# Optimization experiments

Measured on AMD Instinct MI355X. Metric: run time of the kernel, lower is better.

The kernel has to match this reference:

```python
import jax, jax.numpy as jnp
import numpy as np

FLOW_ITERS = 8
DUAL_ITERS = 8
DUAL_STEP = 0.1
DUAL_MOM = 0.9
GRAPH_LAYERS = 2
BIG = 1e9


def _sparsemax(z, mask):
    # sparsemax along last axis; masked entries already hold -BIG, zeroed by mask after.
    V = z.shape[-1]
    zs = jnp.sort(z, axis=-1)[..., ::-1]
    cum = jnp.cumsum(zs, axis=-1)
    k = jnp.arange(1, V + 1, dtype=z.dtype)
    support = zs * k > (cum - 1.0)
    k_sel = jnp.sum(support.astype(jnp.int32), axis=-1, keepdims=True)
    tau = (jnp.take_along_axis(cum, k_sel - 1, axis=-1) - 1.0) / k_sel.astype(z.dtype)
    return jnp.maximum(z - tau, 0.0) * mask


def _min_cost_flow(props, demands):
    # iterative proportional flow routing: push relu(inflow - demand) along predicted proportions
    def body(flow, _):
        inflow = jnp.sum(flow, axis=1)[..., None]      # [B,V,1] inflow to each node
        adjusted = jax.nn.relu(inflow - demands)       # excess to re-route
        return props * adjusted, None                  # row i scaled by its excess
    flow0 = jnp.zeros_like(props)
    flow, _ = jax.lax.scan(body, flow0, None, length=FLOW_ITERS)
    return flow


def _dual_flow(dual_diff, adj):
    # Nesterov-momentum projected gradient on cost(x)=x^2 minus linear dual term, x>=0 on edges
    def body(carry, _):
        flow, acc = carry
        look = flow - DUAL_MOM * acc
        grad = 2.0 * look - dual_diff                  # d/dx x^2 - dual_diff
        acc = DUAL_MOM * acc + DUAL_STEP * grad
        flow = adj * jax.nn.relu(flow - acc)
        return (flow, acc), None
    z = jnp.zeros_like(dual_diff)
    (flow, _), _ = jax.lax.scan(body, (z, z), None, length=DUAL_ITERS)
    return flow


def setup_inputs():
    key = jax.random.key(0)
    ks = jax.random.split(key, 32)
    B, V, F, E, D, K, H = 8, 1200, 8, 16, 64, 2, 4
    node_features = jax.random.normal(ks[0], (B, V, F), dtype=jnp.float32)
    node_embeddings = jax.random.normal(ks[1], (B, V, E), dtype=jnp.float32)
    d = jax.random.normal(ks[2], (B, V, 1), dtype=jnp.float32)
    demands = d - jnp.mean(d, axis=1, keepdims=True)   # balanced supply/demand per graph
    eye = jnp.eye(V, dtype=jnp.float32)
    adj = (jax.random.uniform(ks[3], (B, V, V)) < (16.0 / V)).astype(jnp.float32) * (1.0 - eye)
    hop2 = jnp.clip(adj @ adj, 0.0, 1.0) * (1.0 - eye)
    neighborhoods = jnp.stack([adj, hop2], axis=0)     # [K,B,V,V] k-hop neighborhoods

    def dense(k, fin, fout):
        return (jax.random.normal(k, (fin, fout), dtype=jnp.float32) / np.sqrt(fin)).astype(jnp.float32)

    return dict(
        node_features=node_features, node_embeddings=node_embeddings,
        demands=demands, adj=adj, neighborhoods=neighborhoods,
        enc_w0=dense(ks[4], E + F, D), enc_b0=jnp.zeros((D,), jnp.float32),
        enc_w1=dense(ks[5], D, D), enc_b1=jnp.zeros((D,), jnp.float32),
        agg_w=(jax.random.normal(ks[6], (K, D, D)) / np.sqrt(D)).astype(jnp.float32),
        agg_b=jnp.zeros((K, D), jnp.float32),
        att_w=(jax.random.normal(ks[7], (H, D, D)) / np.sqrt(D)).astype(jnp.float32),
        att_b=jnp.zeros((H, D), jnp.float32),
        att_v=(jax.random.normal(ks[8], (H, D)) / np.sqrt(D)).astype(jnp.float32),
        gru_wu=dense(ks[9], 2 * D, D), gru_bu=jnp.zeros((D,), jnp.float32),
        gru_wr=dense(ks[10], 2 * D, D), gru_br=jnp.zeros((D,), jnp.float32),
        gru_wc=dense(ks[11], 2 * D, D), gru_bc=jnp.zeros((D,), jnp.float32),
        dec_w0=dense(ks[12], D, D), dec_b0=jnp.zeros((D,), jnp.float32),
        dec_w1=dense(ks[13], D, 1), dec_b1=jnp.zeros((1,), jnp.float32),
        dual_w0=dense(ks[14], D, D), dual_b0=jnp.zeros((D,), jnp.float32),
        dual_w1=dense(ks[15], D, 1), dual_b1=jnp.zeros((1,), jnp.float32),
    )


def reference(node_features, node_embeddings, demands, adj, neighborhoods,
              enc_w0, enc_b0, enc_w1, enc_b1, agg_w, agg_b, att_w, att_b, att_v,
              gru_wu, gru_bu, gru_wr, gru_br, gru_wc, gru_bc,
              dec_w0, dec_b0, dec_w1, dec_b1, dual_w0, dual_b0, dual_w1, dual_b1):
    H = att_w.shape[0]
    # node encoder MLP (tanh hidden, tanh final since activate_final=True)
    x = jnp.concatenate([node_embeddings, node_features], axis=-1)
    enc = jnp.tanh(jnp.tanh(x @ enc_w0 + enc_b0) @ enc_w1 + enc_b1)            # [B,V,D]

    deg = jnp.sum(neighborhoods, axis=-1, keepdims=True)
    nb_norm = neighborhoods / jnp.maximum(deg, 1.0)                            # [K,B,V,V]

    for _ in range(GRAPH_LAYERS):
        # per-hop neighborhood aggregation
        msg = jnp.einsum('kbuv,bvd->kbud', nb_norm, enc)
        agg = jnp.tanh(jnp.einsum('kbud,kde->kbue', msg, agg_w) + agg_b[:, None, None, :])
        # multi-head attention over the K hop levels
        proj = jnp.tanh(jnp.einsum('kbvd,hde->hkbve', agg, att_w) + att_b[:, None, None, None, :])
        scores = jnp.einsum('hkbve,he->hkbv', proj, att_v)
        attn = jax.nn.softmax(scores, axis=1)                                  # softmax over hops
        nxt = jnp.einsum('hkbv,kbvd->bvd', attn, agg) / H                      # mean over heads
        # GRU state update
        xs = jnp.concatenate([nxt, enc], axis=-1)
        u = jax.nn.sigmoid(xs @ gru_wu + gru_bu)
        r = jax.nn.sigmoid(xs @ gru_wr + gru_br)
        c = jnp.tanh(jnp.concatenate([nxt, r * enc], axis=-1) @ gru_wc + gru_bc)
        enc = u * enc + (1.0 - u) * c

    # primal: edge weights -> sparsemax -> min-cost-flow
    pred = (enc @ dec_w0 + dec_b0) @ dec_w1 + dec_b1                           # [B,V,1]
    pred_weights = adj * jnp.transpose(pred, (0, 2, 1))                        # [B,V,V]
    weights = -BIG * (1.0 - adj) + pred_weights
    flow_props = _sparsemax(weights, adj)
    flow = _min_cost_flow(flow_props, demands)
    flow_cost = jnp.sum(flow * flow, axis=(1, 2))                              # square cost

    # dual: potentials -> dual-diff -> dual flow solver
    dual = (enc @ dual_w0 + dual_b0) @ dual_w1 + dual_b1                       # [B,V,1]
    dual_diff = adj * (dual - jnp.transpose(dual, (0, 2, 1)))
    dflow = _dual_flow(dual_diff, adj)
    dual_demand = jnp.sum(dual * demands, axis=(1, 2))
    dual_cost = jnp.sum(dflow * dflow - dual_diff * dflow, axis=(1, 2)) - dual_demand

    return flow_cost - dual_cost                                               # duality-gap loss, [B]
```

## Files before the change

kernel.cpp:

```cpp
#include <hip/hip_runtime.h>

#define BB 8
#define VV 1200
#define DD 64
#define KH 2
#define NH 4
#define CAP 64
#define NB2CAP 384
#define NROW (BB*VV)
#define NKROW (KH*BB*VV)

__device__ __forceinline__ float wredsum(float v) {
#pragma unroll
  for (int o = 32; o > 0; o >>= 1) v += __shfl_xor(v, o, 64);
  return v;
}
__device__ __forceinline__ float gredsum32(float v) {
#pragma unroll
  for (int o = 16; o > 0; o >>= 1) v += __shfl_xor(v, o, 64);
  return v;
}

__device__ __forceinline__ float tanh_f(float x) {
  float e = __expf(2.0f * x);
  return 1.0f - 2.0f / (e + 1.0f);
}
__device__ __forceinline__ float sigmoid_f(float x) { return 1.0f / (1.0f + __expf(-x)); }

__device__ __forceinline__ size_t nb_base(int row) {
  return (row < NROW) ? (size_t)row * CAP
                      : (size_t)NROW * CAP + (size_t)(row - NROW) * NB2CAP;
}

#define ENC2B (NROW / 64)
#define CSR2B (NKROW / 8)
__global__ void __launch_bounds__(512) k_pre(
    const float* __restrict__ nb, int* __restrict__ nb_cols, int* __restrict__ nb_cnt,
    const float* __restrict__ emb, const float* __restrict__ feat,
    const float* __restrict__ w0, const float* __restrict__ b0,
    const float* __restrict__ w1, const float* __restrict__ b1,
    float* __restrict__ enc0,
    int* __restrict__ col_cnt, float* __restrict__ out, int out_size) {
  __shared__ float Xe[64][25];
  __shared__ float Ht[64][65];
  __shared__ int colS[8][NB2CAP];
  int bid = blockIdx.x;
  int tid = threadIdx.x;
  if (bid < ENC2B) {
    int tile0 = bid * 64;
    if (tid < 256) {
      int i = tid >> 2, f = tid & 3;
      float4 e4 = *(const float4*)(emb + (size_t)(tile0 + i) * 16 + f * 4);
      Xe[i][f * 4] = e4.x; Xe[i][f * 4 + 1] = e4.y; Xe[i][f * 4 + 2] = e4.z; Xe[i][f * 4 + 3] = e4.w;
    } else if (tid < 384) {
      int t = tid - 256; int i = t >> 1, f = t & 1;
      float4 f4 = *(const float4*)(feat + (size_t)(tile0 + i) * 8 + f * 4);
      Xe[i][16 + f * 4] = f4.x; Xe[i][16 + f * 4 + 1] = f4.y;
      Xe[i][16 + f * 4 + 2] = f4.z; Xe[i][16 + f * 4 + 3] = f4.w;
    }
    __syncthreads();
    int rsub = tid >> 4, cg = tid & 15;
    int c0 = cg * 4, r0 = rsub * 2;
    float a[2][4];
#pragma unroll
    for (int i = 0; i < 2; ++i)
#pragma unroll
      for (int j = 0; j < 4; ++j) a[i][j] = b0[c0 + j];
#pragma unroll
    for (int kk = 0; kk < 24; ++kk) {
      float4 w4 = *(const float4*)(w0 + kk * DD + c0);
      float x0 = Xe[r0][kk], x1 = Xe[r0 + 1][kk];
      a[0][0] = fmaf(x0, w4.x, a[0][0]); a[0][1] = fmaf(x0, w4.y, a[0][1]);
      a[0][2] = fmaf(x0, w4.z, a[0][2]); a[0][3] = fmaf(x0, w4.w, a[0][3]);
      a[1][0] = fmaf(x1, w4.x, a[1][0]); a[1][1] = fmaf(x1, w4.y, a[1][1]);
      a[1][2] = fmaf(x1, w4.z, a[1][2]); a[1][3] = fmaf(x1, w4.w, a[1][3]);
    }
#pragma unroll
    for (int i = 0; i < 2; ++i) {
      Ht[r0 + i][c0] = tanh_f(a[i][0]); Ht[r0 + i][c0 + 1] = tanh_f(a[i][1]);
      Ht[r0 + i][c0 + 2] = tanh_f(a[i][2]); Ht[r0 + i][c0 + 3] = tanh_f(a[i][3]);
    }
    __syncthreads();
    float g[2][4];
#pragma unroll
    for (int i = 0; i < 2; ++i)
#pragma unroll
      for (int j = 0; j < 4; ++j) g[i][j] = b1[c0 + j];
#pragma unroll 8
    for (int kk = 0; kk < DD; ++kk) {
      float4 w4 = *(const float4*)(w1 + kk * DD + c0);
      float x0 = Ht[r0][kk], x1 = Ht[r0 + 1][kk];
      g[0][0] = fmaf(x0, w4.x, g[0][0]); g[0][1] = fmaf(x0, w4.y, g[0][1]);
      g[0][2] = fmaf(x0, w4.z, g[0][2]); g[0][3] = fmaf(x0, w4.w, g[0][3]);
      g[1][0] = fmaf(x1, w4.x, g[1][0]); g[1][1] = fmaf(x1, w4.y, g[1][1]);
      g[1][2] = fmaf(x1, w4.z, g[1][2]); g[1][3] = fmaf(x1, w4.w, g[1][3]);
    }
#pragma unroll
    for (int i = 0; i < 2; ++i) {
      float4 o;
      o.x = tanh_f(g[i][0]); o.y = tanh_f(g[i][1]);
      o.z = tanh_f(g[i][2]); o.w = tanh_f(g[i][3]);
      *(float4*)(enc0 + (size_t)(tile0 + r0 + i) * DD + c0) = o;
    }
  } else if (bid < ENC2B + CSR2B) {
    int w = tid >> 6, lane = tid & 63;
    int row = (bid - ENC2B) * 8 + w;
    const float4* nb4 = (const float4*)(nb + (size_t)row * VV);
    float4 v[5];
#pragma unroll
    for (int c = 0; c < 4; ++c) v[c] = nb4[c * 64 + lane];
    v[4].x = v[4].y = v[4].z = v[4].w = 0.0f;
    if (lane < 44) v[4] = nb4[256 + lane];
    unsigned long long ltmask = (lane == 0) ? 0ull : ((1ull << lane) - 1ull);
    size_t base = nb_base(row);
    int cap = (row < NROW) ? CAP : NB2CAP;
    int off_base = 0;
#pragma unroll
    for (int c = 0; c < 5; ++c) {
      int nz0 = (v[c].x != 0.0f), nz1 = (v[c].y != 0.0f);
      int nz2 = (v[c].z != 0.0f), nz3 = (v[c].w != 0.0f);
      unsigned long long m0 = __ballot(nz0 != 0);
      unsigned long long m1 = __ballot(nz1 != 0);
      unsigned long long m2 = __ballot(nz2 != 0);
      unsigned long long m3 = __ballot(nz3 != 0);
      int lanepref = __popcll(m0 & ltmask) + __popcll(m1 & ltmask)
                   + __popcll(m2 & ltmask) + __popcll(m3 & ltmask);
      int chunkcnt = __popcll(m0) + __popcll(m1) + __popcll(m2) + __popcll(m3);
      int off = off_base + lanepref;
      int vi = (c * 64 + lane) * 4;
      if (nz0 && off < cap) colS[w][off] = vi;
      off += nz0;
      if (nz1 && off < cap) colS[w][off] = vi + 1;
      off += nz1;
      if (nz2 && off < cap) colS[w][off] = vi + 2;
      off += nz2;
      if (nz3 && off < cap) colS[w][off] = vi + 3;
      off_base += chunkcnt;
    }
    int ncp = (off_base > cap) ? cap : off_base;
    if (lane == 0) nb_cnt[row] = ncp;
    for (int j = lane; j < ncp; j += 64) nb_cols[base + j] = colS[w][j];
  } else {
    for (int i = tid; i < NROW; i += 512) col_cnt[i] = 0;
    if (tid < out_size) out[tid] = 0.0f;
  }
}

__global__ void __launch_bounds__(256) k_gather(
    const int* __restrict__ nb_cols, const int* __restrict__ nb_cnt,
    const float* __restrict__ encIn, float* __restrict__ msg) {
  int w = threadIdx.x >> 6, lane = threadIdx.x & 63;
  int row = blockIdx.x * 4 + w;
  int k = (row >= NROW) ? 1 : 0;
  int bv = row - k * NROW;
  int b = bv / VV;
  const float4* encF = (const float4*)(encIn + (size_t)b * VV * DD);
  const int* cols = nb_cols + nb_base(row);
  int n = nb_cnt[row];
  int sub = lane >> 4, q = lane & 15;
  float ax = 0.0f, ay = 0.0f, az = 0.0f, aw = 0.0f;
  int j = 0;
  int cc0 = 0, cc1 = 0, cc2 = 0, cc3 = 0;
  if (j + 16 <= n) {
    cc0 = cols[j + sub]; cc1 = cols[j + 4 + sub];
    cc2 = cols[j + 8 + sub]; cc3 = cols[j + 12 + sub];
  }
  while (j + 16 <= n) {
    int nj = j + 16;
    int p0 = 0, p1 = 0, p2 = 0, p3 = 0;
    if (nj + 16 <= n) {
      p0 = cols[nj + sub]; p1 = cols[nj + 4 + sub];
      p2 = cols[nj + 8 + sub]; p3 = cols[nj + 12 + sub];
    }
    float4 u0 = encF[(size_t)cc0 * 16 + q];
    float4 u1 = encF[(size_t)cc1 * 16 + q];
    float4 u2 = encF[(size_t)cc2 * 16 + q];
    float4 u3 = encF[(size_t)cc3 * 16 + q];
    ax += (u0.x + u1.x) + (u2.x + u3.x);
    ay += (u0.y + u1.y) + (u2.y + u3.y);
    az += (u0.z + u1.z) + (u2.z + u3.z);
    aw += (u0.w + u1.w) + (u2.w + u3.w);
    cc0 = p0; cc1 = p1; cc2 = p2; cc3 = p3;
    j = nj;
  }
  for (; j < n; j += 4) {
    int idx = j + sub;
    if (idx < n) {
      float4 u = encF[(size_t)cols[idx] * 16 + q];
      ax += u.x; ay += u.y; az += u.z; aw += u.w;
    }
  }
#pragma unroll
  for (int o = 16; o < 64; o <<= 1) {
    ax += __shfl_xor(ax, o, 64);
    ay += __shfl_xor(ay, o, 64);
    az += __shfl_xor(az, o, 64);
    aw += __shfl_xor(aw, o, 64);
  }
  if (lane < 16) {
    float inv = 1.0f / fmaxf((float)n, 1.0f);
    float4 r; r.x = ax * inv; r.y = ay * inv; r.z = az * inv; r.w = aw * inv;
    ((float4*)(msg + (size_t)row * DD))[q] = r;
  }
}

__global__ void __launch_bounds__(512) k_mlp(
    const float* __restrict__ msg,
    const float* __restrict__ agg_w, const float* __restrict__ agg_b,
    const float* __restrict__ att_w, const float* __restrict__ att_b,
    const float* __restrict__ att_v,
    float* __restrict__ agg, float* __restrict__ scores) {
  __shared__ float M[64][65];
  __shared__ float G[64][65];
  int tid = threadIdx.x;
  int tile0 = blockIdx.x * 64;
  int k = (tile0 >= NROW) ? 1 : 0;
  int bv0 = tile0 - k * NROW;
  int strip = tid >> 5, cg2 = tid & 31;
  int c0 = cg2 * 2;
  int r0 = strip * 4;
#pragma unroll
  for (int rep = 0; rep < 2; ++rep) {
    int idx = rep * 512 + tid; int i = idx >> 4, d4 = idx & 15;
    float4 m4 = *(const float4*)(msg + (size_t)(tile0 + i) * DD + d4 * 4);
    M[i][d4 * 4] = m4.x; M[i][d4 * 4 + 1] = m4.y; M[i][d4 * 4 + 2] = m4.z; M[i][d4 * 4 + 3] = m4.w;
  }
  __syncthreads();
  const float* W = agg_w + (size_t)k * DD * DD;
  float acc[4][2];
#pragma unroll
  for (int i = 0; i < 4; ++i) {
    acc[i][0] = agg_b[k * DD + c0]; acc[i][1] = agg_b[k * DD + c0 + 1];
  }
#pragma unroll 8
  for (int kk = 0; kk < DD; ++kk) {
    float2 w2 = *(const float2*)(W + kk * DD + c0);
#pragma unroll
    for (int i = 0; i < 4; ++i) {
      float x = M[r0 + i][kk];
      acc[i][0] = fmaf(x, w2.x, acc[i][0]); acc[i][1] = fmaf(x, w2.y, acc[i][1]);
    }
  }
#pragma unroll
  for (int i = 0; i < 4; ++i) {
    float g0 = tanh_f(acc[i][0]), g1 = tanh_f(acc[i][1]);
    G[r0 + i][c0] = g0; G[r0 + i][c0 + 1] = g1;
    *(float2*)(agg + (size_t)(tile0 + r0 + i) * DD + c0) = make_float2(g0, g1);
  }
  __syncthreads();
#pragma unroll
  for (int h = 0; h < NH; ++h) {
    const float* Wh = att_w + (size_t)h * DD * DD;
    float a2[4][2];
#pragma unroll
    for (int i = 0; i < 4; ++i) {
      a2[i][0] = att_b[h * DD + c0]; a2[i][1] = att_b[h * DD + c0 + 1];
    }
#pragma unroll 8
    for (int kk = 0; kk < DD; ++kk) {
      float2 w2 = *(const float2*)(Wh + kk * DD + c0);
#pragma unroll
      for (int i = 0; i < 4; ++i) {
        float x = G[r0 + i][kk];
        a2[i][0] = fmaf(x, w2.x, a2[i][0]); a2[i][1] = fmaf(x, w2.y, a2[i][1]);
      }
    }
    float2 v2 = *(const float2*)(att_v + h * DD + c0);
#pragma unroll
    for (int i = 0; i < 4; ++i) {
      float p = tanh_f(a2[i][0]) * v2.x + tanh_f(a2[i][1]) * v2.y;
      p = gredsum32(p);
      if (cg2 == 0) scores[(size_t)(h * KH + k) * NROW + bv0 + r0 + i] = p;
    }
  }
}

__global__ void __launch_bounds__(128) k_gru(
    const float* __restrict__ encIn, const float* __restrict__ agg,
    const float* __restrict__ scores,
    const float* __restrict__ wu, const float* __restrict__ bu,
    const float* __restrict__ wr, const float* __restrict__ br,
    const float* __restrict__ wc, const float* __restrict__ bc,
    float* __restrict__ encOut,
    int do_decode,
    const float* __restrict__ dw0, const float* __restrict__ db0,
    const float* __restrict__ dw1, const float* __restrict__ db1,
    const float* __restrict__ uw0, const float* __restrict__ ub0,
    const float* __restrict__ uw1, const float* __restrict__ ub1,
    float* __restrict__ pred, float* __restrict__ dualp) {
  __shared__ float X[16][129];
  __shared__ float EO[16][65];
  int tid = threadIdx.x;
  int tile0 = blockIdx.x * 16;
  int strip = tid >> 5, cg2 = tid & 31;
  int c0 = cg2 * 2;
  int r0 = strip * 4;
#pragma unroll
  for (int rep = 0; rep < 2; ++rep) {
    int idx = rep * 128 + tid; int i = idx >> 4, d4 = idx & 15;
    int row = tile0 + i;
    float W0 = 0.0f, W1 = 0.0f;
#pragma unroll
    for (int h = 0; h < NH; ++h) {
      float s0 = scores[(size_t)(h * KH + 0) * NROW + row];
      float s1 = scores[(size_t)(h * KH + 1) * NROW + row];
      float m = fmaxf(s0, s1);
      float e0 = __expf(s0 - m), e1 = __expf(s1 - m);
      float inv = 1.0f / (e0 + e1);
      W0 += e0 * inv; W1 += e1 * inv;
    }
    W0 *= 0.25f; W1 *= 0.25f;
    float4 ef = *(const float4*)(encIn + (size_t)row * DD + d4 * 4);
    float4 a0 = *(const float4*)(agg + (size_t)row * DD + d4 * 4);
    float4 a1 = *(const float4*)(agg + (size_t)(NROW + row) * DD + d4 * 4);
    X[i][d4 * 4]     = W0 * a0.x + W1 * a1.x;
    X[i][d4 * 4 + 1] = W0 * a0.y + W1 * a1.y;
    X[i][d4 * 4 + 2] = W0 * a0.z + W1 * a1.z;
    X[i][d4 * 4 + 3] = W0 * a0.w + W1 * a1.w;
    X[i][64 + d4 * 4]     = ef.x;
    X[i][64 + d4 * 4 + 1] = ef.y;
    X[i][64 + d4 * 4 + 2] = ef.z;
    X[i][64 + d4 * 4 + 3] = ef.w;
  }
  __syncthreads();
  float au[4][2], ar[4][2];
#pragma unroll
  for (int i = 0; i < 4; ++i) {
    au[i][0] = bu[c0]; au[i][1] = bu[c0 + 1];
    ar[i][0] = br[c0]; ar[i][1] = br[c0 + 1];
  }
#pragma unroll 8
  for (int kk = 0; kk < 2 * DD; ++kk) {
    float2 u2 = *(const float2*)(wu + kk * DD + c0);
    float2 r2 = *(const float2*)(wr + kk * DD + c0);
#pragma unroll
    for (int i = 0; i < 4; ++i) {
      float x = X[r0 + i][kk];
      au[i][0] = fmaf(x, u2.x, au[i][0]); au[i][1] = fmaf(x, u2.y, au[i][1]);
      ar[i][0] = fmaf(x, r2.x, ar[i][0]); ar[i][1] = fmaf(x, r2.y, ar[i][1]);
    }
  }
  float uu[4][2], encv[4][2];
#pragma unroll
  for (int i = 0; i < 4; ++i) {
    uu[i][0] = sigmoid_f(au[i][0]); uu[i][1] = sigmoid_f(au[i][1]);
    encv[i][0] = X[r0 + i][64 + c0]; encv[i][1] = X[r0 + i][64 + c0 + 1];
  }
  __syncthreads();
#pragma unroll
  for (int i = 0; i < 4; ++i) {
    X[r0 + i][64 + c0]     = encv[i][0] * sigmoid_f(ar[i][0]);
    X[r0 + i][64 + c0 + 1] = encv[i][1] * sigmoid_f(ar[i][1]);
  }
  __syncthreads();
  float ac[4][2];
#pragma unroll
  for (int i = 0; i < 4; ++i) { ac[i][0] = bc[c0]; ac[i][1] = bc[c0 + 1]; }
#pragma unroll 8
  for (int kk = 0; kk < 2 * DD; ++kk) {
    float2 c2 = *(const float2*)(wc + kk * DD + c0);
#pragma unroll
    for (int i = 0; i < 4; ++i) {
      float x = X[r0 + i][kk];
      ac[i][0] = fmaf(x, c2.x, ac[i][0]); ac[i][1] = fmaf(x, c2.y, ac[i][1]);
    }
  }
#pragma unroll
  for (int i = 0; i < 4; ++i) {
    float e0 = uu[i][0] * encv[i][0] + (1.0f - uu[i][0]) * tanh_f(ac[i][0]);
    float e1 = uu[i][1] * encv[i][1] + (1.0f - uu[i][1]) * tanh_f(ac[i][1]);
    *(float2*)(encOut + (size_t)(tile0 + r0 + i) * DD + c0) = make_float2(e0, e1);
    EO[r0 + i][c0] = e0; EO[r0 + i][c0 + 1] = e1;
  }
  if (do_decode) {
    __syncthreads();
    float hd[4][2], hq[4][2];
#pragma unroll
    for (int i = 0; i < 4; ++i) {
      hd[i][0] = db0[c0]; hd[i][1] = db0[c0 + 1];
      hq[i][0] = ub0[c0]; hq[i][1] = ub0[c0 + 1];
    }
#pragma unroll 8
    for (int kk = 0; kk < DD; ++kk) {
      float2 d2 = *(const float2*)(dw0 + kk * DD + c0);
      float2 q2 = *(const float2*)(uw0 + kk * DD + c0);
#pragma unroll
      for (int i = 0; i < 4; ++i) {
        float x = EO[r0 + i][kk];
        hd[i][0] = fmaf(x, d2.x, hd[i][0]); hd[i][1] = fmaf(x, d2.y, hd[i][1]);
        hq[i][0] = fmaf(x, q2.x, hq[i][0]); hq[i][1] = fmaf(x, q2.y, hq[i][1]);
      }
    }
    float2 dv = *(const float2*)(dw1 + c0);
    float2 qv = *(const float2*)(uw1 + c0);
#pragma unroll
    for (int i = 0; i < 4; ++i) {
      float p = hd[i][0] * dv.x + hd[i][1] * dv.y;
      float q = hq[i][0] * qv.x + hq[i][1] * qv.y;
      p = gredsum32(p);
      q = gredsum32(q);
      if (cg2 == 0) {
        pred[tile0 + r0 + i] = p + db1[0];
        dualp[tile0 + r0 + i] = q + ub1[0];
      }
    }
  }
}

__global__ void __launch_bounds__(256) k_primal_dual(
    const int* __restrict__ nb_cols, const int* __restrict__ nb_cnt,
    const float* __restrict__ pred, const float* __restrict__ dualp,
    const float* __restrict__ dem,
    float* __restrict__ rowsum,
    int* __restrict__ col_cnt, int* __restrict__ col_rows, float* __restrict__ col_vals,
    float* __restrict__ out) {
  __shared__ float bacc[BB];
  if (threadIdx.x < BB) bacc[threadIdx.x] = 0.0f;
  __syncthreads();
  int w = threadIdx.x >> 6, lane = threadIdx.x & 63;
  int row = blockIdx.x * 4 + w;
  int b = row / VV;
  int n = nb_cnt[row];
  int c = (lane < n) ? nb_cols[(size_t)row * CAP + lane] : 0;
  const float* predB = pred + (size_t)b * VV;
  const float* dualB = dualp + (size_t)b * VV;
  float z = (lane < n) ? predB[c] : -1e30f;
  float tau = 0.0f;
  if (n > 0) {
    bool in = (lane < n);
    for (int it = 0; it < 64; ++it) {
      float s = wredsum(in ? z : 0.0f);
      int cnt = (int)__popcll(__ballot(in));
      tau = (s - 1.0f) / (float)cnt;
      bool nin = (z > tau);
      if (__ballot(nin) == __ballot(in)) break;
      in = nin;
    }
  }
  float pv = (lane < n) ? fmaxf(z - tau, 0.0f) : 0.0f;
  float s2 = wredsum(pv * pv);
  if (lane == 0) rowsum[row] = s2;
  if (pv > 0.0f) {
    int g = b * VV + c;
    int j = atomicAdd(&col_cnt[g], 1);
    if (j < CAP) {
      col_rows[(size_t)g * CAP + j] = row - b * VV;
      col_vals[(size_t)g * CAP + j] = pv;
    }
  }
  float du = dualp[row];
  float es = 0.0f;
  if (lane < n) {
    float dd = du - dualB[c];
    float f = 0.0f, acm = 0.0f;
#pragma unroll
    for (int t = 0; t < 8; ++t) {
      float look = f - 0.9f * acm;
      float grad = 2.0f * look - dd;
      acm = 0.9f * acm + 0.1f * grad;
      f = fmaxf(f - acm, 0.0f);
    }
    es = f * f - dd * f;
  }
  float contrib = -es;
  if (lane == 0) contrib += du * dem[row];
  float ws_ = wredsum(contrib);
  if (lane == 0) atomicAdd(&bacc[b], ws_);
  __syncthreads();
  if (threadIdx.x < BB) {
    float t = bacc[threadIdx.x];
    if (t != 0.0f) atomicAdd(&out[threadIdx.x], t);
  }
}

__global__ void __launch_bounds__(1024) k_flow(
    const int* __restrict__ col_cnt, const int* __restrict__ col_rows,
    const float* __restrict__ col_vals, const float* __restrict__ dem,
    const float* __restrict__ rowsum, float* __restrict__ out) {
  __shared__ float aS[VV];
  __shared__ float red[16];
  int b = blockIdx.x;
  int tid = threadIdx.x;
  const float* demB = dem + (size_t)b * VV;
  for (int v = tid; v < VV; v += 1024) aS[v] = fmaxf(-demB[v], 0.0f);
  __syncthreads();
  for (int t = 0; t < 7; ++t) {
    float nv0 = 0.0f, nv1 = 0.0f;
    {
      int v = tid;
      if (v < VV) {
        int g = b * VV + v;
        int n = col_cnt[g]; if (n > CAP) n = CAP;
        const int* cr = col_rows + (size_t)g * CAP;
        const float* cv = col_vals + (size_t)g * CAP;
        float acc = 0.0f;
        for (int j = 0; j < n; ++j) acc += cv[j] * aS[cr[j]];
        nv0 = fmaxf(acc - demB[v], 0.0f);
      }
      v = tid + 1024;
      if (v < VV) {
        int g = b * VV + v;
        int n = col_cnt[g]; if (n > CAP) n = CAP;
        const int* cr = col_rows + (size_t)g * CAP;
        const float* cv = col_vals + (size_t)g * CAP;
        float acc = 0.0f;
        for (int j = 0; j < n; ++j) acc += cv[j] * aS[cr[j]];
        nv1 = fmaxf(acc - demB[v], 0.0f);
      }
    }
    __syncthreads();
    if (tid < VV) aS[tid] = nv0;
    if (tid + 1024 < VV) aS[tid + 1024] = nv1;
    __syncthreads();
  }
  float fc = 0.0f;
  for (int v = tid; v < VV; v += 1024) { float a = aS[v]; fc += a * a * rowsum[b * VV + v]; }
  fc = wredsum(fc);
  int wid = tid >> 6, lane = tid & 63;
  if (lane == 0) red[wid] = fc;
  __syncthreads();
  if (tid == 0) {
    float s = 0.0f;
#pragma unroll
    for (int i = 0; i < 16; ++i) s += red[i];
    atomicAdd(&out[b], s);
  }
}

extern "C" void kernel_launch(void* const* d_in, const int* in_sizes, int n_in,
                              void* d_out, int out_size, void* d_ws, size_t ws_size,
                              hipStream_t stream) {
  const float* feat   = (const float*)d_in[0];
  const float* emb    = (const float*)d_in[1];
  const float* dem    = (const float*)d_in[2];
  const float* nb     = (const float*)d_in[4];
  const float* enc_w0 = (const float*)d_in[5];
  const float* enc_b0 = (const float*)d_in[6];
  const float* enc_w1 = (const float*)d_in[7];
  const float* enc_b1 = (const float*)d_in[8];
  const float* agg_w  = (const float*)d_in[9];
  const float* agg_b  = (const float*)d_in[10];
  const float* att_w  = (const float*)d_in[11];
  const float* att_b  = (const float*)d_in[12];
  const float* att_v  = (const float*)d_in[13];
  const float* gru_wu = (const float*)d_in[14];
  const float* gru_bu = (const float*)d_in[15];
  const float* gru_wr = (const float*)d_in[16];
  const float* gru_br = (const float*)d_in[17];
  const float* gru_wc = (const float*)d_in[18];
  const float* gru_bc = (const float*)d_in[19];
  const float* dec_w0 = (const float*)d_in[20];
  const float* dec_b0 = (const float*)d_in[21];
  const float* dec_w1 = (const float*)d_in[22];
  const float* dec_b1 = (const float*)d_in[23];
  const float* dual_w0= (const float*)d_in[24];
  const float* dual_b0= (const float*)d_in[25];
  const float* dual_w1= (const float*)d_in[26];
  const float* dual_b1= (const float*)d_in[27];
  float* out = (float*)d_out;

  float* enc0 = (float*)d_ws;
  float* enc1 = enc0 + (size_t)NROW * DD;
  float* msg      = enc1 + (size_t)NROW * DD;
  float* aggbuf   = msg + (size_t)NKROW * DD;
  float* scores   = aggbuf + (size_t)NKROW * DD;
  float* pred     = scores + (size_t)NH * KH * NROW;
  float* dualp    = pred + NROW;
  float* rowsum   = dualp + NROW;
  float* col_vals = rowsum + NROW;
  int* col_cnt  = (int*)(col_vals + (size_t)NROW * CAP);
  int* nb_cnt   = col_cnt + NROW;
  int* col_rows = nb_cnt + NKROW;
  int* nb_cols  = col_rows + (size_t)NROW * CAP;

  (void)in_sizes; (void)n_in; (void)ws_size;

  k_pre<<<ENC2B + CSR2B + 1, 512, 0, stream>>>(
      nb, nb_cols, nb_cnt, emb, feat, enc_w0, enc_b0, enc_w1, enc_b1, enc0,
      col_cnt, out, out_size);

  const float* encIn = enc0;
  float* encOut = enc1;
  for (int l = 0; l < 2; ++l) {
    k_gather<<<NKROW / 4, 256, 0, stream>>>(nb_cols, nb_cnt, encIn, msg);
    k_mlp<<<NKROW / 64, 512, 0, stream>>>(msg, agg_w, agg_b, att_w, att_b, att_v,
                                          aggbuf, scores);
    k_gru<<<NROW / 16, 128, 0, stream>>>(encIn, aggbuf, scores,
                                         gru_wu, gru_bu, gru_wr, gru_br, gru_wc, gru_bc,
                                         encOut,
                                         (l == 1) ? 1 : 0,
                                         dec_w0, dec_b0, dec_w1, dec_b1,
                                         dual_w0, dual_b0, dual_w1, dual_b1, pred, dualp);
    const float* t = encIn; encIn = encOut; encOut = (float*)t;
  }

  k_primal_dual<<<NROW / 4, 256, 0, stream>>>(nb_cols, nb_cnt, pred, dualp, dem,
                                              rowsum, col_cnt, col_rows, col_vals, out);
  k_flow<<<BB, 1024, 0, stream>>>(col_cnt, col_rows, col_vals, dem, rowsum, out);
}
```

Baseline: 513.4 us.

## Fuse aggregation MLP, attention scoring and GRU into one per-layer kernel

Merges k_mlp and k_gru into a single k_layer kernel. Each block handles 16 nodes and processes both hop messages, keeping the tanh aggregation outputs and attention scores in shared memory instead of writing them to global buffers and reading them back. This removes one launch per layer and the global round trip of the agg and scores buffers. In exchange, GRU work per thread drops to 2 rows with 256 threads, and weight loads are repeated across more, smaller blocks.

```diff
diff --git a/kernel.cpp b/kernel.cpp
--- a/kernel.cpp
+++ b/kernel.cpp
@@ -204,80 +204,11 @@
   }
 }
 
-__global__ void __launch_bounds__(512) k_mlp(
-    const float* __restrict__ msg,
+__global__ void __launch_bounds__(256) k_layer(
+    const float* __restrict__ msg, const float* __restrict__ encIn,
     const float* __restrict__ agg_w, const float* __restrict__ agg_b,
     const float* __restrict__ att_w, const float* __restrict__ att_b,
     const float* __restrict__ att_v,
-    float* __restrict__ agg, float* __restrict__ scores) {
-  __shared__ float M[64][65];
-  __shared__ float G[64][65];
-  int tid = threadIdx.x;
-  int tile0 = blockIdx.x * 64;
-  int k = (tile0 >= NROW) ? 1 : 0;
-  int bv0 = tile0 - k * NROW;
-  int strip = tid >> 5, cg2 = tid & 31;
-  int c0 = cg2 * 2;
-  int r0 = strip * 4;
-#pragma unroll
-  for (int rep = 0; rep < 2; ++rep) {
-    int idx = rep * 512 + tid; int i = idx >> 4, d4 = idx & 15;
-    float4 m4 = *(const float4*)(msg + (size_t)(tile0 + i) * DD + d4 * 4);
-    M[i][d4 * 4] = m4.x; M[i][d4 * 4 + 1] = m4.y; M[i][d4 * 4 + 2] = m4.z; M[i][d4 * 4 + 3] = m4.w;
-  }
-  __syncthreads();
-  const float* W = agg_w + (size_t)k * DD * DD;
-  float acc[4][2];
-#pragma unroll
-  for (int i = 0; i < 4; ++i) {
-    acc[i][0] = agg_b[k * DD + c0]; acc[i][1] = agg_b[k * DD + c0 + 1];
-  }
-#pragma unroll 8
-  for (int kk = 0; kk < DD; ++kk) {
-    float2 w2 = *(const float2*)(W + kk * DD + c0);
-#pragma unroll
-    for (int i = 0; i < 4; ++i) {
-      float x = M[r0 + i][kk];
-      acc[i][0] = fmaf(x, w2.x, acc[i][0]); acc[i][1] = fmaf(x, w2.y, acc[i][1]);
-    }
-  }
-#pragma unroll
-  for (int i = 0; i < 4; ++i) {
-    float g0 = tanh_f(acc[i][0]), g1 = tanh_f(acc[i][1]);
-    G[r0 + i][c0] = g0; G[r0 + i][c0 + 1] = g1;
-    *(float2*)(agg + (size_t)(tile0 + r0 + i) * DD + c0) = make_float2(g0, g1);
-  }
-  __syncthreads();
-#pragma unroll
-  for (int h = 0; h < NH; ++h) {
-    const float* Wh = att_w + (size_t)h * DD * DD;
-    float a2[4][2];
-#pragma unroll
-    for (int i = 0; i < 4; ++i) {
-      a2[i][0] = att_b[h * DD + c0]; a2[i][1] = att_b[h * DD + c0 + 1];
-    }
-#pragma unroll 8
-    for (int kk = 0; kk < DD; ++kk) {
-      float2 w2 = *(const float2*)(Wh + kk * DD + c0);
-#pragma unroll
-      for (int i = 0; i < 4; ++i) {
-        float x = G[r0 + i][kk];
-        a2[i][0] = fmaf(x, w2.x, a2[i][0]); a2[i][1] = fmaf(x, w2.y, a2[i][1]);
-      }
-    }
-    float2 v2 = *(const float2*)(att_v + h * DD + c0);
-#pragma unroll
-    for (int i = 0; i < 4; ++i) {
-      float p = tanh_f(a2[i][0]) * v2.x + tanh_f(a2[i][1]) * v2.y;
-      p = gredsum32(p);
-      if (cg2 == 0) scores[(size_t)(h * KH + k) * NROW + bv0 + r0 + i] = p;
-    }
-  }
-}
-
-__global__ void __launch_bounds__(128) k_gru(
-    const float* __restrict__ encIn, const float* __restrict__ agg,
-    const float* __restrict__ scores,
     const float* __restrict__ wu, const float* __restrict__ bu,
     const float* __restrict__ wr, const float* __restrict__ br,
     const float* __restrict__ wc, const float* __restrict__ bc,
@@ -288,44 +219,101 @@
     const float* __restrict__ uw0, const float* __restrict__ ub0,
     const float* __restrict__ uw1, const float* __restrict__ ub1,
     float* __restrict__ pred, float* __restrict__ dualp) {
+  __shared__ float M[32][65];
+  __shared__ float G[32][65];
   __shared__ float X[16][129];
   __shared__ float EO[16][65];
+  __shared__ float scS[NH][KH][16];
   int tid = threadIdx.x;
-  int tile0 = blockIdx.x * 16;
+  int t0 = blockIdx.x * 16;
+#pragma unroll
+  for (int rep = 0; rep < 2; ++rep) {
+    int idx = rep * 256 + tid; int i = idx >> 4, d4 = idx & 15;
+    int grow = (i < 16) ? (t0 + i) : (NROW + t0 + (i - 16));
+    float4 m4 = *(const float4*)(msg + (size_t)grow * DD + d4 * 4);
+    M[i][d4 * 4] = m4.x; M[i][d4 * 4 + 1] = m4.y; M[i][d4 * 4 + 2] = m4.z; M[i][d4 * 4 + 3] = m4.w;
+  }
+  __syncthreads();
   int strip = tid >> 5, cg2 = tid & 31;
   int c0 = cg2 * 2;
   int r0 = strip * 4;
-#pragma unroll
-  for (int rep = 0; rep < 2; ++rep) {
-    int idx = rep * 128 + tid; int i = idx >> 4, d4 = idx & 15;
-    int row = tile0 + i;
+  int k = strip >> 2;
+  const float* W = agg_w + (size_t)k * DD * DD;
+  float acc[4][2];
+#pragma unroll
+  for (int i = 0; i < 4; ++i) {
+    acc[i][0] = agg_b[k * DD + c0]; acc[i][1] = agg_b[k * DD + c0 + 1];
+  }
+#pragma unroll 8
+  for (int kk = 0; kk < DD; ++kk) {
+    float2 w2 = *(const float2*)(W + kk * DD + c0);
+#pragma unroll
+    for (int i = 0; i < 4; ++i) {
+      float x = M[r0 + i][kk];
+      acc[i][0] = fmaf(x, w2.x, acc[i][0]); acc[i][1] = fmaf(x, w2.y, acc[i][1]);
+    }
+  }
+#pragma unroll
+  for (int i = 0; i < 4; ++i) {
+    G[r0 + i][c0] = tanh_f(acc[i][0]);
+    G[r0 + i][c0 + 1] = tanh_f(acc[i][1]);
+  }
+  __syncthreads();
+#pragma unroll
+  for (int h = 0; h < NH; ++h) {
+    const float* Wh = att_w + (size_t)h * DD * DD;
+    float a2[4][2];
+#pragma unroll
+    for (int i = 0; i < 4; ++i) {
+      a2[i][0] = att_b[h * DD + c0]; a2[i][1] = att_b[h * DD + c0 + 1];
+    }
+#pragma unroll 8
+    for (int kk = 0; kk < DD; ++kk) {
+      float2 w2 = *(const float2*)(Wh + kk * DD + c0);
+#pragma unroll
+      for (int i = 0; i < 4; ++i) {
+        float x = G[r0 + i][kk];
+        a2[i][0] = fmaf(x, w2.x, a2[i][0]); a2[i][1] = fmaf(x, w2.y, a2[i][1]);
+      }
+    }
+    float2 v2 = *(const float2*)(att_v + h * DD + c0);
+#pragma unroll
+    for (int i = 0; i < 4; ++i) {
+      float p = tanh_f(a2[i][0]) * v2.x + tanh_f(a2[i][1]) * v2.y;
+      p = gredsum32(p);
+      if (cg2 == 0) scS[h][k][(strip & 3) * 4 + i] = p;
+    }
+  }
+  __syncthreads();
+  {
+    int i = tid >> 4, d4 = tid & 15;
     float W0 = 0.0f, W1 = 0.0f;
 #pragma unroll
     for (int h = 0; h < NH; ++h) {
-      float s0 = scores[(size_t)(h * KH + 0) * NROW + row];
-      float s1 = scores[(size_t)(h * KH + 1) * NROW + row];
+      float s0 = scS[h][0][i];
+      float s1 = scS[h][1][i];
       float m = fmaxf(s0, s1);
       float e0 = __expf(s0 - m), e1 = __expf(s1 - m);
       float inv = 1.0f / (e0 + e1);
       W0 += e0 * inv; W1 += e1 * inv;
     }
     W0 *= 0.25f; W1 *= 0.25f;
-    float4 ef = *(const float4*)(encIn + (size_t)row * DD + d4 * 4);
-    float4 a0 = *(const float4*)(agg + (size_t)row * DD + d4 * 4);
-    float4 a1 = *(const float4*)(agg + (size_t)(NROW + row) * DD + d4 * 4);
-    X[i][d4 * 4]     = W0 * a0.x + W1 * a1.x;
-    X[i][d4 * 4 + 1] = W0 * a0.y + W1 * a1.y;
-    X[i][d4 * 4 + 2] = W0 * a0.z + W1 * a1.z;
-    X[i][d4 * 4 + 3] = W0 * a0.w + W1 * a1.w;
+    float4 ef = *(const float4*)(encIn + (size_t)(t0 + i) * DD + d4 * 4);
+#pragma unroll
+    for (int j = 0; j < 4; ++j) {
+      int d = d4 * 4 + j;
+      X[i][d] = W0 * G[i][d] + W1 * G[16 + i][d];
+    }
     X[i][64 + d4 * 4]     = ef.x;
     X[i][64 + d4 * 4 + 1] = ef.y;
     X[i][64 + d4 * 4 + 2] = ef.z;
     X[i][64 + d4 * 4 + 3] = ef.w;
   }
   __syncthreads();
-  float au[4][2], ar[4][2];
-#pragma unroll
-  for (int i = 0; i < 4; ++i) {
+  int gr0 = strip * 2;
+  float au[2][2], ar[2][2];
+#pragma unroll
+  for (int i = 0; i < 2; ++i) {
     au[i][0] = bu[c0]; au[i][1] = bu[c0 + 1];
     ar[i][0] = br[c0]; ar[i][1] = br[c0 + 1];
   }
@@ -334,49 +322,49 @@
     float2 u2 = *(const float2*)(wu + kk * DD + c0);
     float2 r2 = *(const float2*)(wr + kk * DD + c0);
 #pragma unroll
-    for (int i = 0; i < 4; ++i) {
-      float x = X[r0 + i][kk];
+    for (int i = 0; i < 2; ++i) {
+      float x = X[gr0 + i][kk];
       au[i][0] = fmaf(x, u2.x, au[i][0]); au[i][1] = fmaf(x, u2.y, au[i][1]);
       ar[i][0] = fmaf(x, r2.x, ar[i][0]); ar[i][1] = fmaf(x, r2.y, ar[i][1]);
     }
   }
-  float uu[4][2], encv[4][2];
-#pragma unroll
-  for (int i = 0; i < 4; ++i) {
+  float uu[2][2], encv[2][2];
+#pragma unroll
+  for (int i = 0; i < 2; ++i) {
     uu[i][0] = sigmoid_f(au[i][0]); uu[i][1] = sigmoid_f(au[i][1]);
-    encv[i][0] = X[r0 + i][64 + c0]; encv[i][1] = X[r0 + i][64 + c0 + 1];
-  }
-  __syncthreads();
-#pragma unroll
-  for (int i = 0; i < 4; ++i) {
-    X[r0 + i][64 + c0]     = encv[i][0] * sigmoid_f(ar[i][0]);
-    X[r0 + i][64 + c0 + 1] = encv[i][1] * sigmoid_f(ar[i][1]);
-  }
-  __syncthreads();
-  float ac[4][2];
-#pragma unroll
-  for (int i = 0; i < 4; ++i) { ac[i][0] = bc[c0]; ac[i][1] = bc[c0 + 1]; }
+    encv[i][0] = X[gr0 + i][64 + c0]; encv[i][1] = X[gr0 + i][64 + c0 + 1];
+  }
+  __syncthreads();
+#pragma unroll
+  for (int i = 0; i < 2; ++i) {
+    X[gr0 + i][64 + c0]     = encv[i][0] * sigmoid_f(ar[i][0]);
+    X[gr0 + i][64 + c0 + 1] = encv[i][1] * sigmoid_f(ar[i][1]);
+  }
+  __syncthreads();
+  float ac[2][2];
+#pragma unroll
+  for (int i = 0; i < 2; ++i) { ac[i][0] = bc[c0]; ac[i][1] = bc[c0 + 1]; }
 #pragma unroll 8
   for (int kk = 0; kk < 2 * DD; ++kk) {
     float2 c2 = *(const float2*)(wc + kk * DD + c0);
 #pragma unroll
-    for (int i = 0; i < 4; ++i) {
-      float x = X[r0 + i][kk];
+    for (int i = 0; i < 2; ++i) {
+      float x = X[gr0 + i][kk];
       ac[i][0] = fmaf(x, c2.x, ac[i][0]); ac[i][1] = fmaf(x, c2.y, ac[i][1]);
     }
   }
 #pragma unroll
-  for (int i = 0; i < 4; ++i) {
+  for (int i = 0; i < 2; ++i) {
     float e0 = uu[i][0] * encv[i][0] + (1.0f - uu[i][0]) * tanh_f(ac[i][0]);
     float e1 = uu[i][1] * encv[i][1] + (1.0f - uu[i][1]) * tanh_f(ac[i][1]);
-    *(float2*)(encOut + (size_t)(tile0 + r0 + i) * DD + c0) = make_float2(e0, e1);
-    EO[r0 + i][c0] = e0; EO[r0 + i][c0 + 1] = e1;
+    *(float2*)(encOut + (size_t)(t0 + gr0 + i) * DD + c0) = make_float2(e0, e1);
+    EO[gr0 + i][c0] = e0; EO[gr0 + i][c0 + 1] = e1;
   }
   if (do_decode) {
     __syncthreads();
-    float hd[4][2], hq[4][2];
-#pragma unroll
-    for (int i = 0; i < 4; ++i) {
+    float hd[2][2], hq[2][2];
+#pragma unroll
+    for (int i = 0; i < 2; ++i) {
       hd[i][0] = db0[c0]; hd[i][1] = db0[c0 + 1];
       hq[i][0] = ub0[c0]; hq[i][1] = ub0[c0 + 1];
     }
@@ -385,8 +373,8 @@
       float2 d2 = *(const float2*)(dw0 + kk * DD + c0);
       float2 q2 = *(const float2*)(uw0 + kk * DD + c0);
 #pragma unroll
-      for (int i = 0; i < 4; ++i) {
-        float x = EO[r0 + i][kk];
+      for (int i = 0; i < 2; ++i) {
+        float x = EO[gr0 + i][kk];
         hd[i][0] = fmaf(x, d2.x, hd[i][0]); hd[i][1] = fmaf(x, d2.y, hd[i][1]);
         hq[i][0] = fmaf(x, q2.x, hq[i][0]); hq[i][1] = fmaf(x, q2.y, hq[i][1]);
       }
@@ -394,14 +382,14 @@
     float2 dv = *(const float2*)(dw1 + c0);
     float2 qv = *(const float2*)(uw1 + c0);
 #pragma unroll
-    for (int i = 0; i < 4; ++i) {
+    for (int i = 0; i < 2; ++i) {
       float p = hd[i][0] * dv.x + hd[i][1] * dv.y;
       float q = hq[i][0] * qv.x + hq[i][1] * qv.y;
       p = gredsum32(p);
       q = gredsum32(q);
       if (cg2 == 0) {
-        pred[tile0 + r0 + i] = p + db1[0];
-        dualp[tile0 + r0 + i] = q + ub1[0];
+        pred[t0 + gr0 + i] = p + db1[0];
+        dualp[t0 + gr0 + i] = q + ub1[0];
       }
     }
   }
@@ -562,9 +550,7 @@
   float* enc0 = (float*)d_ws;
   float* enc1 = enc0 + (size_t)NROW * DD;
   float* msg      = enc1 + (size_t)NROW * DD;
-  float* aggbuf   = msg + (size_t)NKROW * DD;
-  float* scores   = aggbuf + (size_t)NKROW * DD;
-  float* pred     = scores + (size_t)NH * KH * NROW;
+  float* pred     = msg + (size_t)NKROW * DD;
   float* dualp    = pred + NROW;
   float* rowsum   = dualp + NROW;
   float* col_vals = rowsum + NROW;
@@ -583,14 +569,13 @@
   float* encOut = enc1;
   for (int l = 0; l < 2; ++l) {
     k_gather<<<NKROW / 4, 256, 0, stream>>>(nb_cols, nb_cnt, encIn, msg);
-    k_mlp<<<NKROW / 64, 512, 0, stream>>>(msg, agg_w, agg_b, att_w, att_b, att_v,
-                                          aggbuf, scores);
-    k_gru<<<NROW / 16, 128, 0, stream>>>(encIn, aggbuf, scores,
-                                         gru_wu, gru_bu, gru_wr, gru_br, gru_wc, gru_bc,
-                                         encOut,
-                                         (l == 1) ? 1 : 0,
-                                         dec_w0, dec_b0, dec_w1, dec_b1,
-                                         dual_w0, dual_b0, dual_w1, dual_b1, pred, dualp);
+    k_layer<<<NROW / 16, 256, 0, stream>>>(msg, encIn,
+                                           agg_w, agg_b, att_w, att_b, att_v,
+                                           gru_wu, gru_bu, gru_wr, gru_br, gru_wc, gru_bc,
+                                           encOut,
+                                           (l == 1) ? 1 : 0,
+                                           dec_w0, dec_b0, dec_w1, dec_b1,
+                                           dual_w0, dual_b0, dual_w1, dual_b1, pred, dualp);
     const float* t = encIn; encIn = encOut; encOut = (float*)t;
   }
 
```

After: 514.4 us. No clear change (+0.2%).
